# Performance work log

Measured on AMD Instinct MI355X. Metric: run time of the kernel, lower is better.

Reference implementation:

```python
import jax, jax.numpy as jnp
import numpy as np

B, T, C = 2, 4096, 768
N_HEAD = 12
HEAD_DIM = C // N_HEAD


def setup_inputs() -> dict:
    key = jax.random.key(0)
    k1, k2, k3, k4, k5 = jax.random.split(key, 5)
    scale = 1.0 / np.sqrt(C)
    x = jax.random.normal(k1, (B, T, C), dtype=jnp.float32)
    # weights stored as [in, out] (transpose of torch Linear weight)
    W_attn = jax.random.normal(k2, (C, 3 * C), dtype=jnp.float32) * scale
    b_attn = jax.random.normal(k3, (3 * C,), dtype=jnp.float32) * 0.01
    W_proj = jax.random.normal(k4, (C, C), dtype=jnp.float32) * scale
    b_proj = jax.random.normal(k5, (C,), dtype=jnp.float32) * 0.01
    return {"x": x, "W_attn": W_attn, "b_attn": b_attn, "W_proj": W_proj, "b_proj": b_proj}


def reference(x, W_attn, b_attn, W_proj, b_proj):
    Bq, Tq, Cq = x.shape
    qkv = x @ W_attn + b_attn                      # [B, T, 3C]
    q, k, v = jnp.split(qkv, 3, axis=-1)           # each [B, T, C]

    def heads(t):
        return t.reshape(Bq, Tq, N_HEAD, HEAD_DIM).transpose(0, 2, 1, 3)  # [B, H, T, D]

    q, k, v = heads(q), heads(k), heads(v)
    att = jnp.einsum('bhqd,bhkd->bhqk', q, k) * (1.0 / np.sqrt(HEAD_DIM))  # [B, H, T, T]
    causal = jnp.tril(jnp.ones((Tq, Tq), dtype=bool))                      # [T, T]
    att = jnp.where(causal[None, None], att, jnp.finfo(att.dtype).min)
    att = jax.nn.softmax(att, axis=-1)
    y = jnp.einsum('bhqk,bhkd->bhqd', att, v)      # [B, H, T, D]
    y = y.transpose(0, 2, 1, 3).reshape(Bq, Tq, Cq)
    return y @ W_proj + b_proj
```

## Files before the change

### kernel.cpp

```cpp
#include <hip/hip_runtime.h>


#define TSEQ   4096
#define NHEAD  12
#define CDIM   768
#define C3     2304
#define BT_TOT 8192

#define PSTR   72

typedef __bf16 bf16x8 __attribute__((ext_vector_type(8)));
typedef __bf16 bf16x2 __attribute__((ext_vector_type(2)));
typedef float  f32x4  __attribute__((ext_vector_type(4)));

__device__ __forceinline__ unsigned short f2bf(float f) {
  unsigned int u = __builtin_bit_cast(unsigned int, f);
  u += 0x7FFFu + ((u >> 16) & 1u);
  return (unsigned short)(u >> 16);
}

__device__ __forceinline__ unsigned int pack2bf(float a, float b) {
  bf16x2 v = {(__bf16)a, (__bf16)b};
  return __builtin_bit_cast(unsigned int, v);
}

__device__ __forceinline__ f32x4 mfma16(bf16x8 a, bf16x8 b, f32x4 c) {
  return __builtin_amdgcn_mfma_f32_16x16x32_bf16(a, b, c, 0, 0, 0);
}

typedef const __attribute__((address_space(1))) void* gas_ptr;
typedef __attribute__((address_space(3))) void* las_ptr;

#define LGKM_WAIT() __builtin_amdgcn_s_waitcnt(0xC07F)


__global__ __launch_bounds__(256) void cast_f32_bf16(const float* __restrict__ x,
                                                     unsigned short* __restrict__ o, int n) {
  int i = (blockIdx.x * 256 + threadIdx.x) * 4;
  if (i < n) {
    float4 v = *(const float4*)(x + i);
    ushort4 u;
    u.x = f2bf(v.x); u.y = f2bf(v.y); u.z = f2bf(v.z); u.w = f2bf(v.w);
    *(ushort4*)(o + i) = u;
  }
}

__global__ __launch_bounds__(256) void transpose_cast(const float* __restrict__ src,
                                                      unsigned short* __restrict__ dst,
                                                      int K, int N) {
  __shared__ float tile[32][33];
  int n0 = blockIdx.x * 32, k0 = blockIdx.y * 32;
  int tx = threadIdx.x, ty = threadIdx.y;
#pragma unroll
  for (int i = 0; i < 4; ++i)
    tile[ty + i * 8][tx] = src[(size_t)(k0 + ty + i * 8) * N + n0 + tx];
  __syncthreads();
#pragma unroll
  for (int i = 0; i < 4; ++i)
    dst[(size_t)(n0 + ty + i * 8) * K + k0 + tx] = f2bf(tile[tx][ty + i * 8]);
}


__device__ __forceinline__ void gemm_bt_mainloop(const unsigned short* __restrict__ A,
                                                 const unsigned short* __restrict__ BTm,
                                                 int K, int m0, int n0,
                                                 unsigned short* lds, f32x4 acc[4][4]) {
  const int tid = threadIdx.x;
  const int wave = tid >> 6, lane = tid & 63;
  const int quad = lane >> 4, l16 = lane & 15;
  const int wm = (wave >> 1) * 64, wn = (wave & 1) * 64;
  const int srow = tid >> 2;
  const int scol = (tid & 3) * 8;

  for (int k0 = 0; k0 < K; k0 += 32) {
    __syncthreads();
#pragma unroll
    for (int r = 0; r < 2; ++r) {
      const unsigned short* ga = A + (size_t)(m0 + r * 64 + srow) * K + k0 + scol;
      __builtin_amdgcn_global_load_lds((gas_ptr)ga,
          (las_ptr)(lds + r * 2048 + wave * 512), 16, 0, 0);
      const unsigned short* gb = BTm + (size_t)(n0 + r * 64 + srow) * K + k0 + scol;
      __builtin_amdgcn_global_load_lds((gas_ptr)gb,
          (las_ptr)(lds + 4096 + r * 2048 + wave * 512), 16, 0, 0);
    }
    __syncthreads();

    bf16x8 af[4], bfr[4];
#pragma unroll
    for (int i = 0; i < 4; ++i) {
      af[i]  = *(const bf16x8*)(lds + (wm + i * 16 + l16) * 32 + quad * 8);
      bfr[i] = *(const bf16x8*)(lds + 4096 + (wn + i * 16 + l16) * 32 + quad * 8);
    }
#pragma unroll
    for (int i = 0; i < 4; ++i)
#pragma unroll
      for (int j = 0; j < 4; ++j)
        acc[i][j] = mfma16(af[i], bfr[j], acc[i][j]);
  }
}

__global__ __launch_bounds__(256) void gemm_qkv_kernel(
    const unsigned short* __restrict__ A, const unsigned short* __restrict__ BTm,
    const float* __restrict__ bias,
    unsigned short* __restrict__ qbuf, unsigned short* __restrict__ kbuf,
    unsigned short* __restrict__ vtbuf) {
  __shared__ __align__(16) unsigned short lds[128 * 136];
  f32x4 zero = {0.f, 0.f, 0.f, 0.f};
  f32x4 acc[4][4];
#pragma unroll
  for (int i = 0; i < 4; ++i)
#pragma unroll
    for (int j = 0; j < 4; ++j) acc[i][j] = zero;

  const int m0 = blockIdx.y * 128, n0 = blockIdx.x * 128;
  gemm_bt_mainloop(A, BTm, CDIM, m0, n0, lds, acc);

  const int tid = threadIdx.x;
  const int wave = tid >> 6, lane = tid & 63;
  const int quad = lane >> 4, l16 = lane & 15;
  const int wm = (wave >> 1) * 64, wn = (wave & 1) * 64;
  const float KSCALE = 0.125f * 1.44269504088896340736f;

  const int seg = n0 / CDIM;
  const float mult = (seg == 1) ? KSCALE : 1.0f;

  __syncthreads();
#pragma unroll
  for (int j = 0; j < 4; ++j) {
    const int nl = wn + j * 16 + l16;
    const float bv = bias[n0 + nl];
#pragma unroll
    for (int i = 0; i < 4; ++i) {
#pragma unroll
      for (int r = 0; r < 4; ++r) {
        const int ml = wm + i * 16 + quad * 4 + r;
        unsigned short val = f2bf((acc[i][j][r] + bv) * mult);
        if (seg < 2) lds[ml * 136 + nl] = val;
        else         lds[nl * 136 + ml] = val;
      }
    }
  }
  __syncthreads();

  const int row = tid >> 1, half = tid & 1;
  const unsigned short* src = lds + row * 136 + half * 64;
  unsigned short* dst;
  if (seg < 2) {
    const int m = m0 + row, b = m >> 12, t = m & (TSEQ - 1);
    const int nn = (n0 - seg * CDIM) + half * 64;
    const int h = nn >> 6;
    unsigned short* base = (seg == 0) ? qbuf : kbuf;
    dst = base + ((size_t)(b * NHEAD + h) * TSEQ + t) * 64;
  } else {
    const int nn = (n0 - 2 * CDIM) + row;
    const int h = nn >> 6, d = nn & 63;
    const int b = m0 >> 12, t0 = (m0 & (TSEQ - 1)) + half * 64;
    dst = vtbuf + ((size_t)(b * NHEAD + h) * 64 + d) * TSEQ + t0;
  }
#pragma unroll
  for (int k = 0; k < 8; ++k)
    *(uint4*)(dst + k * 8) = *(const uint4*)(src + k * 8);
}

__global__ __launch_bounds__(256) void gemm_out_kernel(
    const unsigned short* __restrict__ A, const unsigned short* __restrict__ BTm,
    const float* __restrict__ bias, float* __restrict__ out) {
  __shared__ __align__(16) unsigned short lds[8192];
  f32x4 zero = {0.f, 0.f, 0.f, 0.f};
  f32x4 acc[4][4];
#pragma unroll
  for (int i = 0; i < 4; ++i)
#pragma unroll
    for (int j = 0; j < 4; ++j) acc[i][j] = zero;

  const int m0 = blockIdx.y * 128, n0 = blockIdx.x * 128;
  gemm_bt_mainloop(A, BTm, CDIM, m0, n0, lds, acc);

  const int tid = threadIdx.x;
  const int wave = tid >> 6, lane = tid & 63;
  const int quad = lane >> 4, l16 = lane & 15;
  const int wm = (wave >> 1) * 64, wn = (wave & 1) * 64;

#pragma unroll
  for (int j = 0; j < 4; ++j) {
    int n = n0 + wn + j * 16 + l16;
    float bv = bias[n];
#pragma unroll
    for (int i = 0; i < 4; ++i) {
#pragma unroll
      for (int r = 0; r < 4; ++r) {
        int m = m0 + wm + i * 16 + quad * 4 + r;
        out[(size_t)m * CDIM + n] = acc[i][j][r] + bv;
      }
    }
  }
}


__device__ __forceinline__ void stage_kv4(const unsigned short* __restrict__ Kp,
                                          const unsigned short* __restrict__ Vp,
                                          int j0, unsigned short* kb, unsigned short* vb,
                                          int tid, int wave) {
  const int row = tid >> 3;
  const int col = ((tid & 7) ^ (row & 7)) * 8;
  __builtin_amdgcn_global_load_lds((gas_ptr)(Kp + (size_t)(j0 + row) * 64 + col),
                                   (las_ptr)(kb + wave * 512), 16, 0, 0);
  __builtin_amdgcn_global_load_lds((gas_ptr)(Kp + (size_t)(j0 + 32 + row) * 64 + col),
                                   (las_ptr)(kb + 2048 + wave * 512), 16, 0, 0);
  __builtin_amdgcn_global_load_lds((gas_ptr)(Vp + (size_t)row * TSEQ + j0 + col),
                                   (las_ptr)(vb + wave * 512), 16, 0, 0);
  __builtin_amdgcn_global_load_lds((gas_ptr)(Vp + (size_t)(row + 32) * TSEQ + j0 + col),
                                   (las_ptr)(vb + 2048 + wave * 512), 16, 0, 0);
}

__device__ __forceinline__ void qk_score(const bf16x8 kf[8], const bf16x8 qf[2], f32x4 s[4]) {
  f32x4 zero = {0.f, 0.f, 0.f, 0.f};
#pragma unroll
  for (int i = 0; i < 4; ++i)
    s[i] = mfma16(kf[2 * i + 1], qf[1], mfma16(kf[2 * i], qf[0], zero));
}

template <bool MASKED>
__device__ __forceinline__ void exp_write(const f32x4 s[4], unsigned short* __restrict__ prow,
                                          int j0, int q0, int l16, int quad, float& lsum) {
#pragma unroll
  for (int i = 0; i < 4; ++i) {
    float p[4];
#pragma unroll
    for (int r = 0; r < 4; ++r) {
      p[r] = __builtin_amdgcn_exp2f(s[i][r]);
      if (MASKED) {
        if (j0 + i * 16 + quad * 4 + r > q0 + l16) p[r] = 0.f;
      }
      lsum += p[r];
    }
    uint2 w;
    w.x = pack2bf(p[0], p[1]);
    w.y = pack2bf(p[2], p[3]);
    *(uint2*)(prow + l16 * PSTR + i * 16 + quad * 4) = w;
  }
}

__device__ __forceinline__ void pv_dual(const unsigned short* __restrict__ vb, int kcol0,
                                        const unsigned short* __restrict__ p0,
                                        const unsigned short* __restrict__ p1,
                                        int l16, int quad, f32x4 o0[4], f32x4 o1[4]) {
  bf16x8 a00 = *(const bf16x8*)(p0 + l16 * PSTR + quad * 8);
  bf16x8 a01 = *(const bf16x8*)(p0 + l16 * PSTR + 32 + quad * 8);
  bf16x8 a10 = *(const bf16x8*)(p1 + l16 * PSTR + quad * 8);
  bf16x8 a11 = *(const bf16x8*)(p1 + l16 * PSTR + 32 + quad * 8);
#pragma unroll
  for (int dt = 0; dt < 4; ++dt) {
    bf16x8 v0 = *(const bf16x8*)(vb + (16 * dt + l16) * 64 + kcol0);
    bf16x8 v1 = *(const bf16x8*)(vb + (16 * dt + l16) * 64 + (kcol0 ^ 32));
    o0[dt] = mfma16(a01, v1, mfma16(a00, v0, o0[dt]));
    o1[dt] = mfma16(a11, v1, mfma16(a10, v0, o1[dt]));
  }
}

__global__ __launch_bounds__(256, 3) void attn_kernel(const unsigned short* __restrict__ qbuf,
                                                      const unsigned short* __restrict__ kbuf,
                                                      const unsigned short* __restrict__ vtbuf,
                                                      unsigned short* __restrict__ y) {
  __shared__ __align__(16) unsigned short k_lds[2][64 * 64];
  __shared__ __align__(16) unsigned short v_lds[2][64 * 64];
  __shared__ __align__(16) unsigned short p_lds[4][2][16 * PSTR];

  const int tid = threadIdx.x;
  const int wave = tid >> 6, lane = tid & 63;
  const int quad = lane >> 4, l16 = lane & 15;

  const int bh = blockIdx.x % 24;
  const int p = blockIdx.x / 24;
  const bool isA = wave < 2;
  const int qtile = isA ? p : (63 - p);
  const int q0 = qtile * 64 + (wave & 1) * 32;

  const unsigned short* Qp = qbuf + (size_t)bh * TSEQ * 64;
  const unsigned short* Kp = kbuf + (size_t)bh * TSEQ * 64;
  const unsigned short* Vp = vtbuf + (size_t)bh * 64 * TSEQ;
  unsigned short* prow0 = &p_lds[wave][0][0];
  unsigned short* prow1 = &p_lds[wave][1][0];

  bf16x8 qf0[2], qf1[2];
  qf0[0] = *(const bf16x8*)(Qp + (size_t)(q0 + l16) * 64 + quad * 8);
  qf0[1] = *(const bf16x8*)(Qp + (size_t)(q0 + l16) * 64 + 32 + quad * 8);
  qf1[0] = *(const bf16x8*)(Qp + (size_t)(q0 + 16 + l16) * 64 + quad * 8);
  qf1[1] = *(const bf16x8*)(Qp + (size_t)(q0 + 16 + l16) * 64 + 32 + quad * 8);

  f32x4 zero = {0.f, 0.f, 0.f, 0.f};
  f32x4 o0[4], o1[4];
#pragma unroll
  for (int dt = 0; dt < 4; ++dt) { o0[dt] = zero; o1[dt] = zero; }
  float ls0 = 0.f, ls1 = 0.f;

  const int kcol0 = (quad ^ (l16 & 7)) * 8;
  const int ntiles = 64 - p;
  const int lasttile = isA ? p : (ntiles - 1);

  stage_kv4(Kp, Vp, 0, k_lds[0], v_lds[0], tid, wave);

  for (int jt = 0; jt < ntiles; ++jt) {
    __syncthreads();
    if (jt + 1 < ntiles)
      stage_kv4(Kp, Vp, (jt + 1) * 64, k_lds[(jt + 1) & 1], v_lds[(jt + 1) & 1], tid, wave);

    if (jt <= lasttile) {
      const unsigned short* kb = k_lds[jt & 1];
      const unsigned short* vb = v_lds[jt & 1];
      const int j0 = jt * 64;

      bf16x8 kf[8];
#pragma unroll
      for (int i = 0; i < 4; ++i) {
        kf[2 * i]     = *(const bf16x8*)(kb + (16 * i + l16) * 64 + kcol0);
        kf[2 * i + 1] = *(const bf16x8*)(kb + (16 * i + l16) * 64 + (kcol0 ^ 32));
      }

      f32x4 s0[4], s1[4];
      qk_score(kf, qf0, s0);
      qk_score(kf, qf1, s1);
      if (jt == lasttile) {
        exp_write<true>(s0, prow0, j0, q0,      l16, quad, ls0);
        exp_write<true>(s1, prow1, j0, q0 + 16, l16, quad, ls1);
      } else {
        exp_write<false>(s0, prow0, j0, q0,      l16, quad, ls0);
        exp_write<false>(s1, prow1, j0, q0 + 16, l16, quad, ls1);
      }

      LGKM_WAIT();

      pv_dual(vb, kcol0, prow0, prow1, l16, quad, o0, o1);
    }
  }

  ls0 += __shfl_xor(ls0, 16); ls0 += __shfl_xor(ls0, 32);
  ls1 += __shfl_xor(ls1, 16); ls1 += __shfl_xor(ls1, 32);

  const int b = bh / NHEAD, h = bh - b * NHEAD;
#pragma unroll
  for (int r = 0; r < 4; ++r) {
    const int qrow = quad * 4 + r;
    float lq0 = __shfl(ls0, (lane & 48) + qrow);
    float lq1 = __shfl(ls1, (lane & 48) + qrow);
    float inv0 = 1.0f / lq0, inv1 = 1.0f / lq1;
    size_t row0 = (size_t)(b * TSEQ + q0 + qrow) * CDIM + h * 64;
    size_t row1 = (size_t)(b * TSEQ + q0 + 16 + qrow) * CDIM + h * 64;
#pragma unroll
    for (int dt = 0; dt < 4; ++dt) {
      y[row0 + dt * 16 + l16] = f2bf(o0[dt][r] * inv0);
      y[row1 + dt * 16 + l16] = f2bf(o1[dt][r] * inv1);
    }
  }
}


extern "C" void kernel_launch(void* const* d_in, const int* in_sizes, int n_in,
                              void* d_out, int out_size, void* d_ws, size_t ws_size,
                              hipStream_t stream) {
  const float* x      = (const float*)d_in[0];
  const float* W_attn = (const float*)d_in[1];
  const float* b_attn = (const float*)d_in[2];
  const float* W_proj = (const float*)d_in[3];
  const float* b_proj = (const float*)d_in[4];
  float* out = (float*)d_out;

  unsigned short* xb    = (unsigned short*)d_ws;
  unsigned short* WaT   = xb + (size_t)BT_TOT * CDIM;
  unsigned short* WpT   = WaT + (size_t)C3 * CDIM;
  unsigned short* qbuf  = WpT + (size_t)CDIM * CDIM;
  unsigned short* kbuf  = qbuf + (size_t)2 * NHEAD * TSEQ * 64;
  unsigned short* vtbuf = kbuf + (size_t)2 * NHEAD * TSEQ * 64;
  unsigned short* ybuf  = xb;

  cast_f32_bf16<<<(BT_TOT * CDIM) / 1024, 256, 0, stream>>>(x, xb, BT_TOT * CDIM);
  transpose_cast<<<dim3(C3 / 32, CDIM / 32), dim3(32, 8), 0, stream>>>(W_attn, WaT, CDIM, C3);
  transpose_cast<<<dim3(CDIM / 32, CDIM / 32), dim3(32, 8), 0, stream>>>(W_proj, WpT, CDIM, CDIM);

  gemm_qkv_kernel<<<dim3(C3 / 128, BT_TOT / 128), 256, 0, stream>>>(xb, WaT, b_attn,
                                                                    qbuf, kbuf, vtbuf);
  attn_kernel<<<dim3(24 * 32), 256, 0, stream>>>(qbuf, kbuf, vtbuf, ybuf);
  gemm_out_kernel<<<dim3(CDIM / 128, BT_TOT / 128), 256, 0, stream>>>(ybuf, WpT, b_proj, out);
}
```

Measured before the change: 246.1 us.

## Keep softmax probabilities in registers and use 16x16x16 MFMA for PV

The exponentiated score tile is no longer written to LDS and read back as an MFMA operand. The packed bf16 probabilities feed a 16x16x16 bf16 MFMA directly as the B operand, with V read from the swizzled LDS tile as the A operand, so the output comes out transposed. This removes the P round-trip through LDS, the LDS wait and the p_lds allocation, and lets the epilogue write packed 4-element rows without shuffles. In exchange the PV step issues twice as many smaller MFMAs.

```diff
diff --git a/kernel.cpp b/kernel.cpp
--- a/kernel.cpp
+++ b/kernel.cpp
@@ -7,11 +7,10 @@
 #define C3     2304
 #define BT_TOT 8192
 
-#define PSTR   72
-
 typedef __bf16 bf16x8 __attribute__((ext_vector_type(8)));
 typedef __bf16 bf16x2 __attribute__((ext_vector_type(2)));
 typedef float  f32x4  __attribute__((ext_vector_type(4)));
+typedef short  s16x4  __attribute__((ext_vector_type(4)));
 
 __device__ __forceinline__ unsigned short f2bf(float f) {
   unsigned int u = __builtin_bit_cast(unsigned int, f);
@@ -28,10 +27,17 @@
   return __builtin_amdgcn_mfma_f32_16x16x32_bf16(a, b, c, 0, 0, 0);
 }
 
+__device__ __forceinline__ f32x4 mfma16x16(s16x4 a, s16x4 b, f32x4 c) {
+#if defined(__HIP_DEVICE_COMPILE__)
+  return __builtin_amdgcn_mfma_f32_16x16x16bf16_1k(a, b, c, 0, 0, 0);
+#else
+  (void)a; (void)b;
+  return c;
+#endif
+}
+
 typedef const __attribute__((address_space(1))) void* gas_ptr;
 typedef __attribute__((address_space(3))) void* las_ptr;
-
-#define LGKM_WAIT() __builtin_amdgcn_s_waitcnt(0xC07F)
 
 
 __global__ __launch_bounds__(256) void cast_f32_bf16(const float* __restrict__ x,
@@ -221,8 +227,8 @@
 }
 
 template <bool MASKED>
-__device__ __forceinline__ void exp_write(const f32x4 s[4], unsigned short* __restrict__ prow,
-                                          int j0, int q0, int l16, int quad, float& lsum) {
+__device__ __forceinline__ void exp_pack(const f32x4 s[4], s16x4 pf[4],
+                                         int j0, int q0, int l16, int quad, float& lsum) {
 #pragma unroll
   for (int i = 0; i < 4; ++i) {
     float p[4];
@@ -237,24 +243,22 @@
     uint2 w;
     w.x = pack2bf(p[0], p[1]);
     w.y = pack2bf(p[2], p[3]);
-    *(uint2*)(prow + l16 * PSTR + i * 16 + quad * 4) = w;
-  }
-}
-
-__device__ __forceinline__ void pv_dual(const unsigned short* __restrict__ vb, int kcol0,
-                                        const unsigned short* __restrict__ p0,
-                                        const unsigned short* __restrict__ p1,
-                                        int l16, int quad, f32x4 o0[4], f32x4 o1[4]) {
-  bf16x8 a00 = *(const bf16x8*)(p0 + l16 * PSTR + quad * 8);
-  bf16x8 a01 = *(const bf16x8*)(p0 + l16 * PSTR + 32 + quad * 8);
-  bf16x8 a10 = *(const bf16x8*)(p1 + l16 * PSTR + quad * 8);
-  bf16x8 a11 = *(const bf16x8*)(p1 + l16 * PSTR + 32 + quad * 8);
+    pf[i] = __builtin_bit_cast(s16x4, w);
+  }
+}
+
+__device__ __forceinline__ void pv_dual(const unsigned short* __restrict__ vb,
+                                        const int voff[4],
+                                        const s16x4 pf0[4], const s16x4 pf1[4],
+                                        f32x4 o0[4], f32x4 o1[4]) {
 #pragma unroll
   for (int dt = 0; dt < 4; ++dt) {
-    bf16x8 v0 = *(const bf16x8*)(vb + (16 * dt + l16) * 64 + kcol0);
-    bf16x8 v1 = *(const bf16x8*)(vb + (16 * dt + l16) * 64 + (kcol0 ^ 32));
-    o0[dt] = mfma16(a01, v1, mfma16(a00, v0, o0[dt]));
-    o1[dt] = mfma16(a11, v1, mfma16(a10, v0, o1[dt]));
+#pragma unroll
+    for (int i = 0; i < 4; ++i) {
+      s16x4 v = *(const s16x4*)(vb + voff[i] + dt * 1024);
+      o0[dt] = mfma16x16(v, pf0[i], o0[dt]);
+      o1[dt] = mfma16x16(v, pf1[i], o1[dt]);
+    }
   }
 }
 
@@ -264,7 +268,6 @@
                                                       unsigned short* __restrict__ y) {
   __shared__ __align__(16) unsigned short k_lds[2][64 * 64];
   __shared__ __align__(16) unsigned short v_lds[2][64 * 64];
-  __shared__ __align__(16) unsigned short p_lds[4][2][16 * PSTR];
 
   const int tid = threadIdx.x;
   const int wave = tid >> 6, lane = tid & 63;
@@ -279,8 +282,6 @@
   const unsigned short* Qp = qbuf + (size_t)bh * TSEQ * 64;
   const unsigned short* Kp = kbuf + (size_t)bh * TSEQ * 64;
   const unsigned short* Vp = vtbuf + (size_t)bh * 64 * TSEQ;
-  unsigned short* prow0 = &p_lds[wave][0][0];
-  unsigned short* prow1 = &p_lds[wave][1][0];
 
   bf16x8 qf0[2], qf1[2];
   qf0[0] = *(const bf16x8*)(Qp + (size_t)(q0 + l16) * 64 + quad * 8);
@@ -295,6 +296,12 @@
   float ls0 = 0.f, ls1 = 0.f;
 
   const int kcol0 = (quad ^ (l16 & 7)) * 8;
+  const int qh = quad >> 1, x7 = l16 & 7;
+  int voff[4];
+#pragma unroll
+  for (int i = 0; i < 4; ++i)
+    voff[i] = l16 * 64 + (((2 * i + qh) ^ x7) * 8) + (quad & 1) * 4;
+
   const int ntiles = 64 - p;
   const int lasttile = isA ? p : (ntiles - 1);
 
@@ -320,37 +327,36 @@
       f32x4 s0[4], s1[4];
       qk_score(kf, qf0, s0);
       qk_score(kf, qf1, s1);
+
+      s16x4 pf0[4], pf1[4];
       if (jt == lasttile) {
-        exp_write<true>(s0, prow0, j0, q0,      l16, quad, ls0);
-        exp_write<true>(s1, prow1, j0, q0 + 16, l16, quad, ls1);
+        exp_pack<true>(s0, pf0, j0, q0,      l16, quad, ls0);
+        exp_pack<true>(s1, pf1, j0, q0 + 16, l16, quad, ls1);
       } else {
-        exp_write<false>(s0, prow0, j0, q0,      l16, quad, ls0);
-        exp_write<false>(s1, prow1, j0, q0 + 16, l16, quad, ls1);
-      }
-
-      LGKM_WAIT();
-
-      pv_dual(vb, kcol0, prow0, prow1, l16, quad, o0, o1);
+        exp_pack<false>(s0, pf0, j0, q0,      l16, quad, ls0);
+        exp_pack<false>(s1, pf1, j0, q0 + 16, l16, quad, ls1);
+      }
+
+      pv_dual(vb, voff, pf0, pf1, o0, o1);
     }
   }
 
   ls0 += __shfl_xor(ls0, 16); ls0 += __shfl_xor(ls0, 32);
   ls1 += __shfl_xor(ls1, 16); ls1 += __shfl_xor(ls1, 32);
+  const float inv0 = 1.0f / ls0, inv1 = 1.0f / ls1;
 
   const int b = bh / NHEAD, h = bh - b * NHEAD;
-#pragma unroll
-  for (int r = 0; r < 4; ++r) {
-    const int qrow = quad * 4 + r;
-    float lq0 = __shfl(ls0, (lane & 48) + qrow);
-    float lq1 = __shfl(ls1, (lane & 48) + qrow);
-    float inv0 = 1.0f / lq0, inv1 = 1.0f / lq1;
-    size_t row0 = (size_t)(b * TSEQ + q0 + qrow) * CDIM + h * 64;
-    size_t row1 = (size_t)(b * TSEQ + q0 + 16 + qrow) * CDIM + h * 64;
-#pragma unroll
-    for (int dt = 0; dt < 4; ++dt) {
-      y[row0 + dt * 16 + l16] = f2bf(o0[dt][r] * inv0);
-      y[row1 + dt * 16 + l16] = f2bf(o1[dt][r] * inv1);
-    }
+  unsigned short* y0 = y + (size_t)(b * TSEQ + q0 + l16) * CDIM + h * 64 + quad * 4;
+  unsigned short* y1 = y0 + (size_t)16 * CDIM;
+#pragma unroll
+  for (int dt = 0; dt < 4; ++dt) {
+    uint2 w0, w1;
+    w0.x = pack2bf(o0[dt][0] * inv0, o0[dt][1] * inv0);
+    w0.y = pack2bf(o0[dt][2] * inv0, o0[dt][3] * inv0);
+    w1.x = pack2bf(o1[dt][0] * inv1, o1[dt][1] * inv1);
+    w1.y = pack2bf(o1[dt][2] * inv1, o1[dt][3] * inv1);
+    *(uint2*)(y0 + dt * 16) = w0;
+    *(uint2*)(y1 + dt * 16) = w1;
   }
 }
 
```

Result: slower. 252.3 us (+2.5%).

## Switch attention to 32x32x16 MFMA and keep P in registers

Applied to the files above, without the earlier changes.

Rewrites the attention inner loop to use 32x32x16 bf16 MFMA with the score matrix computed transposed (K as the A operand, Q as B). The exponentiated scores then land directly in the register layout needed for the P·V MFMA B operand, so the per-wave P staging through LDS and its waitcnt are removed. V fragments are gathered as two 4-element LDS reads per operand to match the swizzled layout. This cuts LDS traffic and synchronisation, at the cost of larger accumulators and more register pressure, and it relies on the new lane-to-key mapping being correct.

```diff
diff --git a/kernel.cpp b/kernel.cpp
--- a/kernel.cpp
+++ b/kernel.cpp
@@ -7,11 +7,12 @@
 #define C3     2304
 #define BT_TOT 8192
 
-#define PSTR   72
-
 typedef __bf16 bf16x8 __attribute__((ext_vector_type(8)));
+typedef __bf16 bf16x4v __attribute__((ext_vector_type(4)));
 typedef __bf16 bf16x2 __attribute__((ext_vector_type(2)));
 typedef float  f32x4  __attribute__((ext_vector_type(4)));
+typedef float  f32x16 __attribute__((ext_vector_type(16)));
+typedef unsigned int u32x4 __attribute__((ext_vector_type(4)));
 
 __device__ __forceinline__ unsigned short f2bf(float f) {
   unsigned int u = __builtin_bit_cast(unsigned int, f);
@@ -28,10 +29,12 @@
   return __builtin_amdgcn_mfma_f32_16x16x32_bf16(a, b, c, 0, 0, 0);
 }
 
+__device__ __forceinline__ f32x16 mfma32(bf16x8 a, bf16x8 b, f32x16 c) {
+  return __builtin_amdgcn_mfma_f32_32x32x16_bf16(a, b, c, 0, 0, 0);
+}
+
 typedef const __attribute__((address_space(1))) void* gas_ptr;
 typedef __attribute__((address_space(3))) void* las_ptr;
-
-#define LGKM_WAIT() __builtin_amdgcn_s_waitcnt(0xC07F)
 
 
 __global__ __launch_bounds__(256) void cast_f32_bf16(const float* __restrict__ x,
@@ -213,49 +216,26 @@
                                    (las_ptr)(vb + 2048 + wave * 512), 16, 0, 0);
 }
 
-__device__ __forceinline__ void qk_score(const bf16x8 kf[8], const bf16x8 qf[2], f32x4 s[4]) {
-  f32x4 zero = {0.f, 0.f, 0.f, 0.f};
-#pragma unroll
-  for (int i = 0; i < 4; ++i)
-    s[i] = mfma16(kf[2 * i + 1], qf[1], mfma16(kf[2 * i], qf[0], zero));
-}
-
 template <bool MASKED>
-__device__ __forceinline__ void exp_write(const f32x4 s[4], unsigned short* __restrict__ prow,
-                                          int j0, int q0, int l16, int quad, float& lsum) {
-#pragma unroll
-  for (int i = 0; i < 4; ++i) {
-    float p[4];
-#pragma unroll
-    for (int r = 0; r < 4; ++r) {
-      p[r] = __builtin_amdgcn_exp2f(s[i][r]);
-      if (MASKED) {
-        if (j0 + i * 16 + quad * 4 + r > q0 + l16) p[r] = 0.f;
-      }
-      lsum += p[r];
-    }
-    uint2 w;
-    w.x = pack2bf(p[0], p[1]);
-    w.y = pack2bf(p[2], p[3]);
-    *(uint2*)(prow + l16 * PSTR + i * 16 + quad * 4) = w;
-  }
-}
-
-__device__ __forceinline__ void pv_dual(const unsigned short* __restrict__ vb, int kcol0,
-                                        const unsigned short* __restrict__ p0,
-                                        const unsigned short* __restrict__ p1,
-                                        int l16, int quad, f32x4 o0[4], f32x4 o1[4]) {
-  bf16x8 a00 = *(const bf16x8*)(p0 + l16 * PSTR + quad * 8);
-  bf16x8 a01 = *(const bf16x8*)(p0 + l16 * PSTR + 32 + quad * 8);
-  bf16x8 a10 = *(const bf16x8*)(p1 + l16 * PSTR + quad * 8);
-  bf16x8 a11 = *(const bf16x8*)(p1 + l16 * PSTR + 32 + quad * 8);
-#pragma unroll
-  for (int dt = 0; dt < 4; ++dt) {
-    bf16x8 v0 = *(const bf16x8*)(vb + (16 * dt + l16) * 64 + kcol0);
-    bf16x8 v1 = *(const bf16x8*)(vb + (16 * dt + l16) * 64 + (kcol0 ^ 32));
-    o0[dt] = mfma16(a01, v1, mfma16(a00, v0, o0[dt]));
-    o1[dt] = mfma16(a11, v1, mfma16(a10, v0, o1[dt]));
-  }
+__device__ __forceinline__ void exp_pack32(const f32x16 s, int keybase, int qloc, int h,
+                                           float& ls, bf16x8* pf) {
+  unsigned int w[8];
+#pragma unroll
+  for (int pp = 0; pp < 8; ++pp) {
+    float pa = __builtin_amdgcn_exp2f(s[2 * pp]);
+    float pb = __builtin_amdgcn_exp2f(s[2 * pp + 1]);
+    if (MASKED) {
+      const int ka = keybase + 2 * (pp & 1) + 8 * (pp >> 1) + 4 * h;
+      if (ka > qloc)     pa = 0.f;
+      if (ka + 1 > qloc) pb = 0.f;
+    }
+    ls += pa + pb;
+    w[pp] = pack2bf(pa, pb);
+  }
+  u32x4 lo = {w[0], w[1], w[2], w[3]};
+  u32x4 hi = {w[4], w[5], w[6], w[7]};
+  pf[0] = __builtin_bit_cast(bf16x8, lo);
+  pf[1] = __builtin_bit_cast(bf16x8, hi);
 }
 
 __global__ __launch_bounds__(256, 3) void attn_kernel(const unsigned short* __restrict__ qbuf,
@@ -264,37 +244,33 @@
                                                       unsigned short* __restrict__ y) {
   __shared__ __align__(16) unsigned short k_lds[2][64 * 64];
   __shared__ __align__(16) unsigned short v_lds[2][64 * 64];
-  __shared__ __align__(16) unsigned short p_lds[4][2][16 * PSTR];
 
   const int tid = threadIdx.x;
   const int wave = tid >> 6, lane = tid & 63;
-  const int quad = lane >> 4, l16 = lane & 15;
+  const int l31 = lane & 31, h = lane >> 5;
+  const int x7 = l31 & 7;
 
   const int bh = blockIdx.x % 24;
   const int p = blockIdx.x / 24;
   const bool isA = wave < 2;
   const int qtile = isA ? p : (63 - p);
   const int q0 = qtile * 64 + (wave & 1) * 32;
+  const int qloc = (wave & 1) * 32 + l31;
 
   const unsigned short* Qp = qbuf + (size_t)bh * TSEQ * 64;
   const unsigned short* Kp = kbuf + (size_t)bh * TSEQ * 64;
   const unsigned short* Vp = vtbuf + (size_t)bh * 64 * TSEQ;
-  unsigned short* prow0 = &p_lds[wave][0][0];
-  unsigned short* prow1 = &p_lds[wave][1][0];
-
-  bf16x8 qf0[2], qf1[2];
-  qf0[0] = *(const bf16x8*)(Qp + (size_t)(q0 + l16) * 64 + quad * 8);
-  qf0[1] = *(const bf16x8*)(Qp + (size_t)(q0 + l16) * 64 + 32 + quad * 8);
-  qf1[0] = *(const bf16x8*)(Qp + (size_t)(q0 + 16 + l16) * 64 + quad * 8);
-  qf1[1] = *(const bf16x8*)(Qp + (size_t)(q0 + 16 + l16) * 64 + 32 + quad * 8);
-
-  f32x4 zero = {0.f, 0.f, 0.f, 0.f};
-  f32x4 o0[4], o1[4];
-#pragma unroll
-  for (int dt = 0; dt < 4; ++dt) { o0[dt] = zero; o1[dt] = zero; }
-  float ls0 = 0.f, ls1 = 0.f;
-
-  const int kcol0 = (quad ^ (l16 & 7)) * 8;
+
+  bf16x8 qf[4];
+#pragma unroll
+  for (int dg = 0; dg < 4; ++dg)
+    qf[dg] = *(const bf16x8*)(Qp + (size_t)(q0 + l31) * 64 + dg * 16 + h * 8);
+
+  const f32x16 zero16 = {0.f, 0.f, 0.f, 0.f, 0.f, 0.f, 0.f, 0.f,
+                         0.f, 0.f, 0.f, 0.f, 0.f, 0.f, 0.f, 0.f};
+  f32x16 o0 = zero16, o1 = zero16;
+  float ls = 0.f;
+
   const int ntiles = 64 - p;
   const int lasttile = isA ? p : (ntiles - 1);
 
@@ -308,49 +284,55 @@
     if (jt <= lasttile) {
       const unsigned short* kb = k_lds[jt & 1];
       const unsigned short* vb = v_lds[jt & 1];
-      const int j0 = jt * 64;
-
-      bf16x8 kf[8];
-#pragma unroll
-      for (int i = 0; i < 4; ++i) {
-        kf[2 * i]     = *(const bf16x8*)(kb + (16 * i + l16) * 64 + kcol0);
-        kf[2 * i + 1] = *(const bf16x8*)(kb + (16 * i + l16) * 64 + (kcol0 ^ 32));
-      }
-
-      f32x4 s0[4], s1[4];
-      qk_score(kf, qf0, s0);
-      qk_score(kf, qf1, s1);
+
+      bf16x8 kf0[4], kf1[4];
+#pragma unroll
+      for (int dg = 0; dg < 4; ++dg) {
+        kf0[dg] = *(const bf16x8*)(kb + (size_t)l31 * 64        + ((2 * dg + h) ^ x7) * 8);
+        kf1[dg] = *(const bf16x8*)(kb + (size_t)(32 + l31) * 64 + ((2 * dg + h) ^ x7) * 8);
+      }
+      f32x16 s0 = zero16, s1 = zero16;
+#pragma unroll
+      for (int dg = 0; dg < 4; ++dg) {
+        s0 = mfma32(kf0[dg], qf[dg], s0);
+        s1 = mfma32(kf1[dg], qf[dg], s1);
+      }
+
+      bf16x8 pf[4];
       if (jt == lasttile) {
-        exp_write<true>(s0, prow0, j0, q0,      l16, quad, ls0);
-        exp_write<true>(s1, prow1, j0, q0 + 16, l16, quad, ls1);
+        exp_pack32<true>(s0, 0,  qloc, h, ls, &pf[0]);
+        exp_pack32<true>(s1, 32, qloc, h, ls, &pf[2]);
       } else {
-        exp_write<false>(s0, prow0, j0, q0,      l16, quad, ls0);
-        exp_write<false>(s1, prow1, j0, q0 + 16, l16, quad, ls1);
-      }
-
-      LGKM_WAIT();
-
-      pv_dual(vb, kcol0, prow0, prow1, l16, quad, o0, o1);
-    }
-  }
-
-  ls0 += __shfl_xor(ls0, 16); ls0 += __shfl_xor(ls0, 32);
-  ls1 += __shfl_xor(ls1, 16); ls1 += __shfl_xor(ls1, 32);
-
-  const int b = bh / NHEAD, h = bh - b * NHEAD;
-#pragma unroll
-  for (int r = 0; r < 4; ++r) {
-    const int qrow = quad * 4 + r;
-    float lq0 = __shfl(ls0, (lane & 48) + qrow);
-    float lq1 = __shfl(ls1, (lane & 48) + qrow);
-    float inv0 = 1.0f / lq0, inv1 = 1.0f / lq1;
-    size_t row0 = (size_t)(b * TSEQ + q0 + qrow) * CDIM + h * 64;
-    size_t row1 = (size_t)(b * TSEQ + q0 + 16 + qrow) * CDIM + h * 64;
-#pragma unroll
-    for (int dt = 0; dt < 4; ++dt) {
-      y[row0 + dt * 16 + l16] = f2bf(o0[dt][r] * inv0);
-      y[row1 + dt * 16 + l16] = f2bf(o1[dt][r] * inv1);
-    }
+        exp_pack32<false>(s0, 0,  qloc, h, ls, &pf[0]);
+        exp_pack32<false>(s1, 32, qloc, h, ls, &pf[2]);
+      }
+
+      const unsigned short* vr0 = vb + (size_t)l31 * 64;
+      const unsigned short* vr1 = vb + (size_t)(32 + l31) * 64;
+#pragma unroll
+      for (int kgg = 0; kgg < 4; ++kgg) {
+        const int c0 = ((2 * kgg)     ^ x7) * 8 + 4 * h;
+        const int c1 = ((2 * kgg + 1) ^ x7) * 8 + 4 * h;
+        bf16x4v a0 = *(const bf16x4v*)(vr0 + c0);
+        bf16x4v b0 = *(const bf16x4v*)(vr0 + c1);
+        bf16x4v a1 = *(const bf16x4v*)(vr1 + c0);
+        bf16x4v b1 = *(const bf16x4v*)(vr1 + c1);
+        o0 = mfma32(__builtin_shufflevector(a0, b0, 0, 1, 2, 3, 4, 5, 6, 7), pf[kgg], o0);
+        o1 = mfma32(__builtin_shufflevector(a1, b1, 0, 1, 2, 3, 4, 5, 6, 7), pf[kgg], o1);
+      }
+    }
+  }
+
+  ls += __shfl_xor(ls, 32);
+  const float inv = 1.0f / ls;
+
+  const int b = bh / NHEAD, hd = bh - b * NHEAD;
+  unsigned short* yr = y + (size_t)(b * TSEQ + q0 + l31) * CDIM + hd * 64;
+#pragma unroll
+  for (int pp = 0; pp < 8; ++pp) {
+    const int d = 2 * (pp & 1) + 8 * (pp >> 1) + 4 * h;
+    *(unsigned int*)(yr + d)      = pack2bf(o0[2 * pp] * inv, o0[2 * pp + 1] * inv);
+    *(unsigned int*)(yr + 32 + d) = pack2bf(o1[2 * pp] * inv, o1[2 * pp + 1] * inv);
   }
 }
 
```

Measured after the change: 248.5 us. No clear change (+1.0%).
